# Kernel optimization log

Measured on AMD Instinct MI355X. Metric: run time of the kernel, lower is better.

Reference implementation:

```python
import jax, jax.numpy as jnp
import numpy as np

B, LD, LQ = 32, 512, 32
E, NF = 300, 4
D = E + NF            # doc_input_size = 304
M = 16                # fofe_max_length == max_len
ALPHA = 0.9
VOCAB = 50000
H = 256
SAMPLE_NUM = 256
POS_N = 128           # int(sample_num * (1 - neg_ratio))
NEG_N = SAMPLE_NUM - POS_N
R = min(M, LD - 2)    # candidate negative lengths = 16
PPL = NEG_N // R + 1  # negatives drawn per length = 9


def setup_inputs() -> dict:
    key = jax.random.key(0)
    ks = jax.random.split(key, 16)
    emb = jax.random.normal(ks[0], (VOCAB, E), jnp.float32) * 0.1
    emb = emb.at[0].set(0.0)  # padding_idx=0
    doc = jax.random.randint(ks[1], (B, LD), 1, VOCAB)
    doc_f = jax.random.normal(ks[2], (B, LD, NF), jnp.float32) * 0.1
    query = jax.random.randint(ks[3], (B, LQ), 1, VOCAB)
    target_s = jax.random.randint(ks[4], (B,), 1, LD - M - 2)
    span = jax.random.randint(ks[5], (B,), 0, M)  # ans_span = target_e - target_s < fofe_max_length
    target_e = target_s + span
    rand_length = jax.random.permutation(ks[6], R)  # torch.randperm(min(max_len, L-2))
    # rand_position[i] ~ randint(1, LD - rand_length[i] - 1)
    u = jax.random.uniform(ks[7], (R, PPL))
    size = (LD - rand_length - 2).astype(jnp.float32)[:, None]
    rand_position = 1 + jnp.floor(u * size).astype(jnp.int32)
    rand_idx = jax.random.randint(ks[8], (NEG_N,), 0, B)  # faithful to original (dim-0 size used as bound)
    perm_idx = jax.random.permutation(ks[9], SAMPLE_NUM)

    def w(k, o, i):
        return jax.random.normal(k, (o, i), jnp.float32) * (1.0 / np.sqrt(i))

    CIN = 3 * D + E  # 1212
    W1 = w(ks[10], 4 * H, CIN)
    W2 = w(ks[11], 4 * H, 4 * H)
    W3 = w(ks[12], 4 * H, 4 * H)
    W4 = w(ks[13], 2 * H, 4 * H)
    W5 = w(ks[14], 1, 2 * H)
    doc_mask = jnp.zeros((B, LD), bool)
    query_mask = jnp.zeros((B, LQ), bool)
    return dict(doc=doc, doc_f=doc_f, query=query, target_s=target_s, target_e=target_e,
                doc_mask=doc_mask, query_mask=query_mask, emb=emb,
                W1=W1, W2=W2, W3=W3, W4=W4, W5=W5,
                rand_length=rand_length, rand_position=rand_position,
                rand_idx=rand_idx, perm_idx=perm_idx)


def _fofe_codes(x):
    """x: [B, D, LD] -> forward/inverse FOFE codes [B, D, M, LD].
    fwd[b,c,l,t] = sum_{k=0}^{l} alpha^k x[b,c,t-k]; inv mirrors to the right."""
    fwd_terms = jnp.stack(
        [(ALPHA ** k) * jnp.pad(x, ((0, 0), (0, 0), (k, 0)))[..., :LD] for k in range(M)], axis=2)
    inv_terms = jnp.stack(
        [(ALPHA ** k) * jnp.pad(x, ((0, 0), (0, 0), (0, k)))[..., k:] for k in range(M)], axis=2)
    return jnp.cumsum(fwd_terms, axis=2), jnp.cumsum(inv_terms, axis=2)


def _cnn(x, W1, W2, W3, W4, W5):
    h = jax.nn.relu(jnp.einsum('oi,bis->bos', W1, x))
    h = jax.nn.relu(jnp.einsum('oi,bis->bos', W2, h))
    h = jax.nn.relu(jnp.einsum('oi,bis->bos', W3, h))
    h = jax.nn.relu(jnp.einsum('oi,bis->bos', W4, h))
    return jax.nn.sigmoid(jnp.einsum('oi,bis->bos', W5, h))


def reference(doc, doc_f, query, target_s, target_e, doc_mask, query_mask, emb,
              W1, W2, W3, W4, W5, rand_length, rand_position, rand_idx, perm_idx):
    # input_embedding (dropout_emb = 0, pos/ner disabled)
    doc_input = jnp.concatenate([emb[doc], doc_f], axis=-1)  # [B, LD, D]
    x = jnp.swapaxes(doc_input, 1, 2)                         # [B, D, LD]
    fwd, inv = _fofe_codes(x)                                 # [B, D, M, LD] each

    # --- positive samples: gold span + left/right full contexts ---
    b = jnp.arange(B)
    span = target_e - target_s
    ans = fwd[b, :, span, target_e]                               # [B, D]
    l_ctx = fwd[b, :, M - 1, jnp.maximum(target_s - 1, 0)]        # [B, D]
    r_ctx = inv[b, :, M - 1, jnp.minimum(target_e + 1, LD - 1)]   # [B, D]
    pos = jnp.concatenate([l_ctx, ans, r_ctx], axis=-1)          # [B, 3D]
    pos = jnp.broadcast_to(pos[:, :, None], (B, 3 * D, POS_N))

    # --- negative samples: random spans of each length in rand_length ---
    rl = rand_length[:, None]                                     # [R, 1]
    neg_ans = fwd[:, :, rl, rand_position].reshape(B, D, R * PPL)
    neg_l = fwd[:, :, M - 1, rand_position - 1].reshape(B, D, R * PPL)
    neg_r = inv[:, :, M - 1, rand_position + rl + 1].reshape(B, D, R * PPL)
    rand_cat = jnp.concatenate([neg_l, neg_ans, neg_r], axis=1)   # [B, 3D, R*PPL]
    neg = rand_cat[:, :, rand_idx]                                # [B, 3D, NEG_N]

    # --- shuffle pos+neg, build query FOFE, run cnn, mse (sum) loss ---
    ctx_ans = jnp.concatenate([pos, neg], axis=-1)[:, :, perm_idx]
    target = jnp.concatenate(
        [jnp.ones((B, 1, POS_N), jnp.float32), jnp.zeros((B, 1, NEG_N), jnp.float32)],
        axis=-1)[:, :, perm_idx]
    qw = ALPHA ** jnp.arange(LQ - 1, -1, -1, dtype=jnp.float32)   # fofe_linear weights
    qf = jnp.einsum('t,bte->be', qw, emb[query])                  # [B, E]
    qb = jnp.broadcast_to(qf[:, :, None], (B, E, SAMPLE_NUM))
    dq_input = jnp.concatenate([ctx_ans, qb], axis=1)             # [B, 3D+E, S]
    score = _cnn(dq_input, W1, W2, W3, W4, W5)                    # [B, 1, S]
    loss = jnp.sum((score - target) ** 2)                         # mse_loss(size_average=False)
    return loss
```

## Files before the change

kernel.cpp:

```cpp
#include <hip/hip_runtime.h>
#include <hip/hip_bf16.h>

#define B_    32
#define LD_   512
#define LQ_   32
#define E_    300
#define NF_   4
#define D_    304
#define M_    16
#define ALPHA_ 0.9f
#define CIN_  1212
#define KP1_  1280
#define NCOL_ 1056
#define NPAD_ 1088
#define PPL_  9
#define NEG_N_ 128

typedef short short8 __attribute__((ext_vector_type(8)));
typedef float f32x4 __attribute__((ext_vector_type(4)));

__device__ __forceinline__ unsigned short f2bf(float f) {
    unsigned int x = __float_as_uint(f);
    unsigned int r = (x + 0x7FFFu + ((x >> 16) & 1u)) >> 16;
    return (unsigned short)r;
}

__global__ __launch_bounds__(320) void prep(
    const int* __restrict__ doc, const float* __restrict__ doc_f,
    const int* __restrict__ query,
    const int* __restrict__ target_s, const int* __restrict__ target_e,
    const float* __restrict__ emb,
    const int* __restrict__ rand_length, const int* __restrict__ rand_position,
    const float* __restrict__ W1,
    unsigned short* __restrict__ W1b,
    unsigned short* __restrict__ Ft, float* __restrict__ zbuf,
    unsigned* __restrict__ done)
{
    int bid = blockIdx.x;
    int tid = threadIdx.x;

    if (bid < NCOL_) {
        int b = bid / 33;
        int col = bid % 33;
        __shared__ int   s_t[3][16];
        __shared__ float s_w[3][16];
        __shared__ int   s_row[3][16];
        if (tid < 48) {
            int part = tid >> 4, k = tid & 15;
            int t; float valid;
            if (col == 0) {
                int ts = target_s[b], te = target_e[b];
                int span = te - ts;
                if (part == 0)      { t = ts - 1 - k;  valid = (t >= 0) ? 1.f : 0.f; }
                else if (part == 1) { t = te - k;      valid = (k <= span && t >= 0) ? 1.f : 0.f; }
                else                { t = te + 1 + k;  valid = (t < LD_) ? 1.f : 0.f; }
            } else {
                int j = col - 1;
                int r = j / PPL_, p = j - r * PPL_;
                int rl = rand_length[r];
                int rp = rand_position[r * PPL_ + p];
                if (part == 0)      { t = rp - 1 - k;      valid = (t >= 0) ? 1.f : 0.f; }
                else if (part == 1) { t = rp - k;          valid = (k <= rl && t >= 0) ? 1.f : 0.f; }
                else                { t = rp + rl + 1 + k; valid = (t < LD_) ? 1.f : 0.f; }
            }
            float w = (valid != 0.f) ? powf(ALPHA_, (float)k) : 0.f;
            t = min(max(t, 0), LD_ - 1);
            s_t[part][k] = t;
            s_w[part][k] = w;
            s_row[part][k] = doc[b * LD_ + t];
        }
        __syncthreads();

        unsigned short* out = Ft + (size_t)bid * KP1_;
        int g = tid;
        if (g < 228) {
            int part = g / 76;
            int g2 = g - part * 76;
            int cc = g2 * 4;
            float ax = 0.f, ay = 0.f, az = 0.f, aw = 0.f;
            if (cc < 300) {
                for (int i = 0; i < 16; ++i) {
                    float4 v = *(const float4*)(emb + (size_t)s_row[part][i] * E_ + cc);
                    float wv = s_w[part][i];
                    ax += wv * v.x; ay += wv * v.y; az += wv * v.z; aw += wv * v.w;
                }
            } else {
                for (int i = 0; i < 16; ++i) {
                    float4 v = *(const float4*)(doc_f + ((size_t)b * LD_ + s_t[part][i]) * NF_);
                    float wv = s_w[part][i];
                    ax += wv * v.x; ay += wv * v.y; az += wv * v.z; aw += wv * v.w;
                }
            }
            ushort4 o; o.x = f2bf(ax); o.y = f2bf(ay); o.z = f2bf(az); o.w = f2bf(aw);
            *(ushort4*)(out + 4 * g) = o;
        } else if (g < 303) {
            if (col == 0) {
                int ce = (g - 228) * 4;
                float ax = 0.f, ay = 0.f, az = 0.f, aw = 0.f;
                float wv = powf(ALPHA_, (float)(LQ_ - 1));
                for (int i = 0; i < 32; ++i) {
                    int row = query[b * LQ_ + i];
                    float4 v = *(const float4*)(emb + (size_t)row * E_ + ce);
                    ax += wv * v.x; ay += wv * v.y; az += wv * v.z; aw += wv * v.w;
                    wv *= (1.0f / ALPHA_);
                }
                ushort4 o; o.x = f2bf(ax); o.y = f2bf(ay); o.z = f2bf(az); o.w = f2bf(aw);
                for (int j = 0; j < 33; ++j)
                    *(ushort4*)(Ft + (size_t)(bid + j) * KP1_ + 4 * g) = o;
            }
        } else {
            ushort4 z; z.x = 0; z.y = 0; z.z = 0; z.w = 0;
            *(ushort4*)(out + 4 * g) = z;
        }
    } else if (bid < 2080) {
        long i = (long)(bid - NCOL_) * 320L + tid;
        long m = i / 320; int k4 = (int)(i - m * 320);
        ushort4 o;
        if (k4 < 303) {
            float4 v = *(const float4*)(W1 + m * CIN_ + k4 * 4);
            o.x = f2bf(v.x); o.y = f2bf(v.y); o.z = f2bf(v.z); o.w = f2bf(v.w);
        } else { o.x = 0; o.y = 0; o.z = 0; o.w = 0; }
        *(ushort4*)(W1b + i * 4) = o;
    } else if (bid < 2112) {
        int row = NCOL_ + (bid - 2080);
        ushort4 z; z.x = 0; z.y = 0; z.z = 0; z.w = 0;
        *(ushort4*)(Ft + (size_t)row * KP1_ + tid * 4) = z;
    } else {
        for (int i = tid; i < NPAD_; i += 320) zbuf[i] = 0.f;
        if (tid < 8) done[tid] = 0u;
    }
}

struct GemmS { unsigned short A[2][64][72]; unsigned short B[2][64][72]; };

__device__ __forceinline__ void gemm_core(
    const unsigned short* __restrict__ A,
    const unsigned short* __restrict__ Bm,
    int K, int m0, int n0, GemmS& sh, f32x4 acc[4])
{
    int tid = threadIdx.x;
    int w = tid >> 6, lane = tid & 63;
    int wm = (w >> 1) * 32, wn = (w & 1) * 32;
    int lr = tid >> 2;
    int ls = (tid & 3) * 16;
    int fr = lane & 15, fk = (lane >> 4) * 8;

    const unsigned short* Arow = A + (size_t)(m0 + lr) * K + ls;
    const unsigned short* Brow = Bm + (size_t)(n0 + lr) * K + ls;

    #pragma unroll
    for (int t = 0; t < 4; ++t) { acc[t][0]=0.f; acc[t][1]=0.f; acc[t][2]=0.f; acc[t][3]=0.f; }

    int nk = K >> 6;
    *(uint4*)&sh.A[0][lr][ls]     = *(const uint4*)(Arow);
    *(uint4*)&sh.A[0][lr][ls + 8] = *(const uint4*)(Arow + 8);
    *(uint4*)&sh.B[0][lr][ls]     = *(const uint4*)(Brow);
    *(uint4*)&sh.B[0][lr][ls + 8] = *(const uint4*)(Brow + 8);
    __syncthreads();
    int cur = 0;
    for (int i = 0; i < nk; ++i) {
        uint4 na0, na1, nb0, nb1;
        bool more = (i + 1 < nk);
        if (more) {
            const unsigned short* An = Arow + (size_t)(i + 1) * 64;
            const unsigned short* Bn = Brow + (size_t)(i + 1) * 64;
            na0 = *(const uint4*)(An);
            na1 = *(const uint4*)(An + 8);
            nb0 = *(const uint4*)(Bn);
            nb1 = *(const uint4*)(Bn + 8);
        }
        #pragma unroll
        for (int s = 0; s < 2; ++s) {
            short8 fa0 = *(const short8*)&sh.A[cur][wm + fr][s * 32 + fk];
            short8 fa1 = *(const short8*)&sh.A[cur][wm + 16 + fr][s * 32 + fk];
            short8 fb0 = *(const short8*)&sh.B[cur][wn + fr][s * 32 + fk];
            short8 fb1 = *(const short8*)&sh.B[cur][wn + 16 + fr][s * 32 + fk];
            acc[0] = __builtin_amdgcn_mfma_f32_16x16x32_bf16(fa0, fb0, acc[0], 0, 0, 0);
            acc[1] = __builtin_amdgcn_mfma_f32_16x16x32_bf16(fa0, fb1, acc[1], 0, 0, 0);
            acc[2] = __builtin_amdgcn_mfma_f32_16x16x32_bf16(fa1, fb0, acc[2], 0, 0, 0);
            acc[3] = __builtin_amdgcn_mfma_f32_16x16x32_bf16(fa1, fb1, acc[3], 0, 0, 0);
        }
        if (more) {
            int nb = cur ^ 1;
            *(uint4*)&sh.A[nb][lr][ls]     = na0;
            *(uint4*)&sh.A[nb][lr][ls + 8] = na1;
            *(uint4*)&sh.B[nb][lr][ls]     = nb0;
            *(uint4*)&sh.B[nb][lr][ls + 8] = nb1;
        }
        __syncthreads();
        cur ^= 1;
    }
}

__global__ __launch_bounds__(256) void gemm_relu(
    const unsigned short* __restrict__ A,
    const unsigned short* __restrict__ Bm,
    unsigned short* __restrict__ C, int M, int K,
    const float* __restrict__ Wn, unsigned short* __restrict__ Wnb,
    int conv_groups)
{
    __shared__ GemmS sh;
    int bid = blockIdx.x;
    int tid = threadIdx.x;
    if (bid >= 272) {
        for (long i = (long)(bid - 272) * 256 + tid; i < conv_groups;
             i += 64L * 256) {
            float4 v = *(const float4*)(Wn + i * 4);
            ushort4 o;
            o.x = f2bf(v.x); o.y = f2bf(v.y); o.z = f2bf(v.z); o.w = f2bf(v.w);
            *(ushort4*)(Wnb + i * 4) = o;
        }
        return;
    }
    int m0 = (bid & 15) * 64, n0 = (bid >> 4) * 64;
    f32x4 acc[4];
    gemm_core(A, Bm, K, m0, n0, sh, acc);
    int w = tid >> 6, lane = tid & 63;
    int wm = (w >> 1) * 32, wn = (w & 1) * 32;
    int rbase = (lane >> 4) * 4;
    int cb = lane & 15;
    #pragma unroll
    for (int t = 0; t < 4; ++t) {
        int MT = t >> 1, NT = t & 1;
        int m = m0 + wm + MT * 16 + rbase;
        int n = n0 + wn + NT * 16 + cb;
        ushort4 o;
        o.x = f2bf(fmaxf(acc[t][0], 0.f));
        o.y = f2bf(fmaxf(acc[t][1], 0.f));
        o.z = f2bf(fmaxf(acc[t][2], 0.f));
        o.w = f2bf(fmaxf(acc[t][3], 0.f));
        *(ushort4*)(C + (size_t)n * M + m) = o;
    }
}

__global__ __launch_bounds__(256) void gemm4_score_loss(
    const unsigned short* __restrict__ A,
    const unsigned short* __restrict__ Bm,
    const float* __restrict__ W5, const int* __restrict__ rand_idx,
    float* __restrict__ zbuf, unsigned* __restrict__ done,
    float* __restrict__ out, int M, int K)
{
    __shared__ GemmS sh;
    __shared__ int s_flag;
    __shared__ int s_cnt[32];
    __shared__ float s_red[256];
    int m0 = blockIdx.x * 64, n0 = blockIdx.y * 64;
    f32x4 acc[4];
    gemm_core(A, Bm, K, m0, n0, sh, acc);
    int tid = threadIdx.x;
    int w = tid >> 6, lane = tid & 63;
    int wm = (w >> 1) * 32, wn = (w & 1) * 32;
    int fr = lane & 15, fq = lane >> 4;
    #pragma unroll
    for (int NT = 0; NT < 2; ++NT) {
        float p = 0.f;
        #pragma unroll
        for (int MT = 0; MT < 2; ++MT) {
            const f32x4 a = acc[MT * 2 + NT];
            int mb = m0 + wm + MT * 16 + fq * 4;
            p += fmaxf(a[0], 0.f) * W5[mb]
               + fmaxf(a[1], 0.f) * W5[mb + 1]
               + fmaxf(a[2], 0.f) * W5[mb + 2]
               + fmaxf(a[3], 0.f) * W5[mb + 3];
        }
        p += __shfl_down(p, 32);
        p += __shfl_down(p, 16);
        if (fq == 0) {
            int n = n0 + wn + NT * 16 + fr;
            atomicAdd(&zbuf[n], p);
        }
    }
    __syncthreads();
    if (tid == 0) {
        unsigned old = __hip_atomic_fetch_add(done, 1u, __ATOMIC_ACQ_REL,
                                              __HIP_MEMORY_SCOPE_AGENT);
        s_flag = (old == 8 * 17 - 1) ? 1 : 0;
    }
    __syncthreads();
    if (s_flag) {
        if (tid < 32) s_cnt[tid] = 0;
        __syncthreads();
        if (tid < NEG_N_) atomicAdd(&s_cnt[rand_idx[tid]], 1);
        __syncthreads();
        float accv = 0.f;
        for (int c = tid; c < NCOL_; c += 256) {
            float z = __hip_atomic_load(&zbuf[c], __ATOMIC_ACQUIRE,
                                        __HIP_MEMORY_SCOPE_AGENT);
            float s = 1.f / (1.f + expf(-z));
            int c33 = c % 33;
            if (c33 == 0) { float d = s - 1.f; accv += 128.f * d * d; }
            else          { accv += (float)s_cnt[c33 - 1] * s * s; }
        }
        s_red[tid] = accv;
        __syncthreads();
        for (int o = 128; o > 0; o >>= 1) {
            if (tid < o) s_red[tid] += s_red[tid + o];
            __syncthreads();
        }
        if (tid == 0) out[0] = s_red[0];
    }
}

extern "C" void kernel_launch(void* const* d_in, const int* in_sizes, int n_in,
                              void* d_out, int out_size, void* d_ws, size_t ws_size,
                              hipStream_t stream)
{
    const int*   doc        = (const int*)d_in[0];
    const float* doc_f      = (const float*)d_in[1];
    const int*   query      = (const int*)d_in[2];
    const int*   target_s   = (const int*)d_in[3];
    const int*   target_e   = (const int*)d_in[4];
    const float* emb        = (const float*)d_in[7];
    const float* W1         = (const float*)d_in[8];
    const float* W2         = (const float*)d_in[9];
    const float* W3         = (const float*)d_in[10];
    const float* W4         = (const float*)d_in[11];
    const float* W5         = (const float*)d_in[12];
    const int*   rand_length   = (const int*)d_in[13];
    const int*   rand_position = (const int*)d_in[14];
    const int*   rand_idx      = (const int*)d_in[15];

    char* ws = (char*)d_ws;
    size_t off = 0;
    auto alloc = [&](size_t bytes) {
        void* p = ws + off;
        off = (off + bytes + 255) & ~(size_t)255;
        return p;
    };
    unsigned short* W1b = (unsigned short*)alloc((size_t)1024 * KP1_ * 2);
    unsigned short* W2b = (unsigned short*)alloc((size_t)1024 * 1024 * 2);
    unsigned short* W3b = (unsigned short*)alloc((size_t)1024 * 1024 * 2);
    unsigned short* W4b = (unsigned short*)alloc((size_t)512 * 1024 * 2);
    unsigned short* Ft  = (unsigned short*)alloc((size_t)NPAD_ * KP1_ * 2);
    unsigned short* hA  = (unsigned short*)alloc((size_t)NPAD_ * 1024 * 2);
    unsigned short* hB  = (unsigned short*)alloc((size_t)NPAD_ * 1024 * 2);
    float*    zbuf      = (float*)alloc((size_t)NPAD_ * sizeof(float));
    unsigned* done      = (unsigned*)alloc(256);
    (void)ws_size; (void)in_sizes; (void)n_in; (void)out_size;

    prep<<<dim3(2113), dim3(320), 0, stream>>>(
        doc, doc_f, query, target_s, target_e, emb,
        rand_length, rand_position,
        W1, W1b, Ft, zbuf, done);

    gemm_relu<<<dim3(336), dim3(256), 0, stream>>>(
        W1b, Ft, hA, 1024, KP1_, W2, W2b, 262144);
    gemm_relu<<<dim3(336), dim3(256), 0, stream>>>(
        W2b, hA, hB, 1024, 1024, W3, W3b, 262144);
    gemm_relu<<<dim3(336), dim3(256), 0, stream>>>(
        W3b, hB, hA, 1024, 1024, W4, W4b, 131072);
    gemm4_score_loss<<<dim3(8, 17), dim3(256), 0, stream>>>(
        W4b, hA, W5, rand_idx, zbuf, done, (float*)d_out, 512, 1024);
}
```

Baseline: 186.8 us.

## Stage per-batch document embeddings in shared memory for FOFE feature prep

```diff
diff --git a/kernel.cpp b/kernel.cpp
--- a/kernel.cpp
+++ b/kernel.cpp
@@ -39,81 +39,95 @@
     int bid = blockIdx.x;
     int tid = threadIdx.x;
 
-    if (bid < NCOL_) {
-        int b = bid / 33;
-        int col = bid % 33;
-        __shared__ int   s_t[3][16];
-        __shared__ float s_w[3][16];
-        __shared__ int   s_row[3][16];
-        if (tid < 48) {
-            int part = tid >> 4, k = tid & 15;
-            int t; float valid;
-            if (col == 0) {
-                int ts = target_s[b], te = target_e[b];
-                int span = te - ts;
-                if (part == 0)      { t = ts - 1 - k;  valid = (t >= 0) ? 1.f : 0.f; }
-                else if (part == 1) { t = te - k;      valid = (k <= span && t >= 0) ? 1.f : 0.f; }
-                else                { t = te + 1 + k;  valid = (t < LD_) ? 1.f : 0.f; }
-            } else {
-                int j = col - 1;
-                int r = j / PPL_, p = j - r * PPL_;
-                int rl = rand_length[r];
-                int rp = rand_position[r * PPL_ + p];
-                if (part == 0)      { t = rp - 1 - k;      valid = (t >= 0) ? 1.f : 0.f; }
-                else if (part == 1) { t = rp - k;          valid = (k <= rl && t >= 0) ? 1.f : 0.f; }
-                else                { t = rp + rl + 1 + k; valid = (t < LD_) ? 1.f : 0.f; }
-            }
-            float w = (valid != 0.f) ? powf(ALPHA_, (float)k) : 0.f;
-            t = min(max(t, 0), LD_ - 1);
-            s_t[part][k] = t;
-            s_w[part][k] = w;
-            s_row[part][k] = doc[b * LD_ + t];
-        }
-        __syncthreads();
-
-        unsigned short* out = Ft + (size_t)bid * KP1_;
-        int g = tid;
-        if (g < 228) {
-            int part = g / 76;
-            int g2 = g - part * 76;
-            int cc = g2 * 4;
-            float ax = 0.f, ay = 0.f, az = 0.f, aw = 0.f;
-            if (cc < 300) {
-                for (int i = 0; i < 16; ++i) {
-                    float4 v = *(const float4*)(emb + (size_t)s_row[part][i] * E_ + cc);
-                    float wv = s_w[part][i];
-                    ax += wv * v.x; ay += wv * v.y; az += wv * v.z; aw += wv * v.w;
+    if (bid < 320) {
+        int b = bid / 10, slice = bid - b * 10;
+        int ch0 = slice * 32;
+        __shared__ float Ds[512][32];
+        __shared__ float Qs[32][32];
+        __shared__ float Qacc[32];
+        __shared__ int   s_doc[512];
+        __shared__ float s_aw[16];
+
+        for (int r = tid; r < 512; r += 320) s_doc[r] = doc[b * LD_ + r];
+        if (tid < 16) s_aw[tid] = powf(ALPHA_, (float)tid);
+        __syncthreads();
+
+        if (slice < 9) {
+            for (int idx = tid; idx < 512 * 8; idx += 320) {
+                int r = idx >> 3, f = idx & 7;
+                *(float4*)&Ds[r][f * 4] =
+                    *(const float4*)(emb + (size_t)s_doc[r] * E_ + ch0 + f * 4);
+            }
+            for (int idx = tid; idx < 32 * 8; idx += 320) {
+                int r = idx >> 3, f = idx & 7;
+                *(float4*)&Qs[r][f * 4] =
+                    *(const float4*)(emb + (size_t)query[b * LQ_ + r] * E_ + ch0 + f * 4);
+            }
+        } else {
+            for (int idx = tid; idx < 512 * 3; idx += 320) {
+                int r = idx / 3, f = idx - r * 3;
+                *(float4*)&Ds[r][f * 4] =
+                    *(const float4*)(emb + (size_t)s_doc[r] * E_ + ch0 + f * 4);
+            }
+            for (int r = tid; r < 512; r += 320)
+                *(float4*)&Ds[r][12] =
+                    *(const float4*)(doc_f + ((size_t)b * LD_ + r) * NF_);
+            for (int idx = tid; idx < 32 * 3; idx += 320) {
+                int r = idx / 3, f = idx - r * 3;
+                *(float4*)&Qs[r][f * 4] =
+                    *(const float4*)(emb + (size_t)query[b * LQ_ + r] * E_ + ch0 + f * 4);
+            }
+        }
+        __syncthreads();
+
+        int c = tid & 31, slot = tid >> 5;
+        int ts = target_s[b], te = target_e[b];
+        for (int round = 0; round < 10; ++round) {
+            int jp = round * 10 + slot;
+            if (jp < 99) {
+                int j = jp / 3, part = jp - j * 3;
+                int A, kl;
+                if (j == 0) { A = (part == 0) ? ts : te; kl = te - ts; }
+                else {
+                    int jj = j - 1, r = jj / PPL_, p = jj - r * PPL_;
+                    int rl = rand_length[r], rp = rand_position[r * PPL_ + p];
+                    A = (part == 2) ? (rp + rl) : rp; kl = rl;
                 }
-            } else {
-                for (int i = 0; i < 16; ++i) {
-                    float4 v = *(const float4*)(doc_f + ((size_t)b * LD_ + s_t[part][i]) * NF_);
-                    float wv = s_w[part][i];
-                    ax += wv * v.x; ay += wv * v.y; az += wv * v.z; aw += wv * v.w;
+                float acc = 0.f;
+                #pragma unroll
+                for (int k = 0; k < 16; ++k) {
+                    int t; float valid;
+                    if (part == 0)      { t = A - 1 - k; valid = (t >= 0) ? 1.f : 0.f; }
+                    else if (part == 1) { t = A - k;     valid = (k <= kl && t >= 0) ? 1.f : 0.f; }
+                    else                { t = A + 1 + k; valid = (t < LD_) ? 1.f : 0.f; }
+                    t = min(max(t, 0), LD_ - 1);
+                    acc += (valid * s_aw[k]) * Ds[t][c];
                 }
-            }
-            ushort4 o; o.x = f2bf(ax); o.y = f2bf(ay); o.z = f2bf(az); o.w = f2bf(aw);
-            *(ushort4*)(out + 4 * g) = o;
-        } else if (g < 303) {
-            if (col == 0) {
-                int ce = (g - 228) * 4;
-                float ax = 0.f, ay = 0.f, az = 0.f, aw = 0.f;
-                float wv = powf(ALPHA_, (float)(LQ_ - 1));
-                for (int i = 0; i < 32; ++i) {
-                    int row = query[b * LQ_ + i];
-                    float4 v = *(const float4*)(emb + (size_t)row * E_ + ce);
-                    ax += wv * v.x; ay += wv * v.y; az += wv * v.z; aw += wv * v.w;
-                    wv *= (1.0f / ALPHA_);
-                }
-                ushort4 o; o.x = f2bf(ax); o.y = f2bf(ay); o.z = f2bf(az); o.w = f2bf(aw);
-                for (int j = 0; j < 33; ++j)
-                    *(ushort4*)(Ft + (size_t)(bid + j) * KP1_ + 4 * g) = o;
-            }
-        } else {
-            ushort4 z; z.x = 0; z.y = 0; z.z = 0; z.w = 0;
-            *(ushort4*)(out + 4 * g) = z;
-        }
-    } else if (bid < 2080) {
-        long i = (long)(bid - NCOL_) * 320L + tid;
+                if (ch0 + c < 304)
+                    Ft[(size_t)(b * 33 + j) * KP1_ + part * 304 + ch0 + c] = f2bf(acc);
+            }
+        }
+
+        if (slot == 0) {
+            float qa = 0.f, wv = powf(ALPHA_, (float)(LQ_ - 1));
+            for (int i = 0; i < 32; ++i) { qa += wv * Qs[i][c]; wv *= (1.0f / ALPHA_); }
+            Qacc[c] = qa;
+        }
+        __syncthreads();
+        if (ch0 + c < 300) {
+            unsigned short qb = f2bf(Qacc[c]);
+            for (int j = slot; j < 33; j += 10)
+                Ft[(size_t)(b * 33 + j) * KP1_ + 912 + ch0 + c] = qb;
+        }
+        if (slice == 0) {
+            for (int idx = tid; idx < 33 * 17; idx += 320) {
+                int j = idx / 17, u = idx - j * 17;
+                ushort4 z; z.x = 0; z.y = 0; z.z = 0; z.w = 0;
+                *(ushort4*)(Ft + (size_t)(b * 33 + j) * KP1_ + 1212 + u * 4) = z;
+            }
+        }
+    } else if (bid < 1344) {
+        long i = (long)(bid - 320) * 320L + tid;
         long m = i / 320; int k4 = (int)(i - m * 320);
         ushort4 o;
         if (k4 < 303) {
@@ -121,8 +135,8 @@
             o.x = f2bf(v.x); o.y = f2bf(v.y); o.z = f2bf(v.z); o.w = f2bf(v.w);
         } else { o.x = 0; o.y = 0; o.z = 0; o.w = 0; }
         *(ushort4*)(W1b + i * 4) = o;
-    } else if (bid < 2112) {
-        int row = NCOL_ + (bid - 2080);
+    } else if (bid < 1376) {
+        int row = NCOL_ + (bid - 1344);
         ushort4 z; z.x = 0; z.y = 0; z.z = 0; z.w = 0;
         *(ushort4*)(Ft + (size_t)row * KP1_ + tid * 4) = z;
     } else {
@@ -338,7 +352,7 @@
     unsigned* done      = (unsigned*)alloc(256);
     (void)ws_size; (void)in_sizes; (void)n_in; (void)out_size;
 
-    prep<<<dim3(2113), dim3(320), 0, stream>>>(
+    prep<<<dim3(1377), dim3(320), 0, stream>>>(
         doc, doc_f, query, target_s, target_e, emb,
         rand_length, rand_position,
         W1, W1b, Ft, zbuf, done);
```

New measurement: 246.4 us. 31.9% more time.
